# Kernel tuning notes

Measured on AMD Instinct MI355X. Metric: run time of the kernel, lower is better.

## Reference

```python
import jax, jax.numpy as jnp
import numpy as np

N_HEAD = 12


def setup_inputs() -> dict:
    key = jax.random.key(0)
    k1, k2, k3 = jax.random.split(key, 3)
    B, S, D = 4, 2048, 768
    x = jax.random.normal(k1, (B, S, D), dtype=jnp.float32)
    std = 0.02
    w_attn = jax.random.normal(k2, (D, 3 * D), dtype=jnp.float32) * std
    b_attn = jnp.zeros((3 * D,), dtype=jnp.float32)
    w_proj = jax.random.normal(k3, (D, D), dtype=jnp.float32) * std
    b_proj = jnp.zeros((D,), dtype=jnp.float32)
    return {"x": x, "w_attn": w_attn, "b_attn": b_attn,
            "w_proj": w_proj, "b_proj": b_proj}


def reference(x, w_attn, b_attn, w_proj, b_proj):
    B, S, D = x.shape
    H = N_HEAD
    hd = D // H
    # c_attn: [B,S,3D]
    qkv = jnp.einsum('bsd,de->bse', x, w_attn) + b_attn
    q, k, v = jnp.split(qkv, 3, axis=2)
    # split heads -> [B,H,S,hd]
    q = q.reshape(B, S, H, hd).transpose(0, 2, 1, 3)
    k = k.reshape(B, S, H, hd).transpose(0, 2, 1, 3)
    v = v.reshape(B, S, H, hd).transpose(0, 2, 1, 3)
    # scores [B,H,S,S]; scale=False in original default
    w = jnp.einsum('bhqd,bhkd->bhqk', q, k)
    # original mask trick: w*b + 1e-9*(1-b), b = lower-triangular ones
    mask = jnp.tril(jnp.ones((S, S), dtype=w.dtype))
    w = w * mask + 1e-9 * (1 - mask)
    w = jax.nn.softmax(w, axis=-1)
    a = jnp.einsum('bhqk,bhkd->bhqd', w, v)
    # merge heads -> [B,S,D]
    a = a.transpose(0, 2, 1, 3).reshape(B, S, D)
    # c_proj
    out = jnp.einsum('bsd,de->bse', a, w_proj) + b_proj
    return out
```

## Files before the change

kernel.cpp:

```cpp
#include <hip/hip_runtime.h>
#include <cstdint>

typedef unsigned short u16;
typedef __bf16 bf16;
typedef bf16 bf16x8 __attribute__((ext_vector_type(8)));
typedef u16 u16x4 __attribute__((ext_vector_type(4)));
typedef u16 u16x8 __attribute__((ext_vector_type(8)));
typedef float f32x4 __attribute__((ext_vector_type(4)));

__device__ __forceinline__ u16 f2b(float f) {
    return __builtin_bit_cast(u16, (bf16)f);
}
__device__ __forceinline__ float b2f(u16 u) {
    return __uint_as_float(((unsigned)u) << 16);
}
__device__ __forceinline__ void load_lds16(const void* g, void* l) {
    auto gp = reinterpret_cast<const __attribute__((address_space(1))) void*>(
        reinterpret_cast<uintptr_t>(g));
    auto lp = reinterpret_cast<__attribute__((address_space(3))) void*>(
        reinterpret_cast<uintptr_t>(l));
    __builtin_amdgcn_global_load_lds(gp, lp, 16, 0, 0);
}
__device__ __forceinline__ f32x4 mfma16(bf16x8 a, bf16x8 b, f32x4 c) {
    return __builtin_amdgcn_mfma_f32_16x16x32_bf16(a, b, c, 0, 0, 0);
}

__global__ __launch_bounds__(256) void convx_kernel(const float* __restrict__ x,
                                                    u16* __restrict__ xb, int n4) {
    int i = blockIdx.x * blockDim.x + threadIdx.x;
    int stride = gridDim.x * blockDim.x;
    for (; i < n4; i += stride) {
        float4 v = ((const float4*)x)[i];
        u16x4 r;
        r[0] = f2b(v.x); r[1] = f2b(v.y); r[2] = f2b(v.z); r[3] = f2b(v.w);
        *(u16x4*)&xb[(size_t)i * 4] = r;
    }
}

__global__ __launch_bounds__(256) void wtrans2_kernel(const float* __restrict__ wa,
                                                      const float* __restrict__ wp,
                                                      u16* __restrict__ wTa,
                                                      u16* __restrict__ wTp) {
    __shared__ float tile[32][33];
    const int bx = blockIdx.x;
    const float* w;
    u16* wT;
    int N, n0;
    if (bx < 72) { w = wa; wT = wTa; N = 2304; n0 = bx * 32; }
    else         { w = wp; wT = wTp; N = 768;  n0 = (bx - 72) * 32; }
    const int K = 768;
    int tx = threadIdx.x, ty = threadIdx.y;
    int k0 = blockIdx.y * 32;
#pragma unroll
    for (int i = 0; i < 4; ++i)
        tile[ty + i * 8][tx] = w[(size_t)(k0 + ty + i * 8) * N + n0 + tx];
    __syncthreads();
#pragma unroll
    for (int i = 0; i < 4; ++i)
        wT[(size_t)(n0 + ty + i * 8) * K + k0 + tx] = f2b(tile[tx][ty + i * 8]);
}

template <bool OUT_BF16>
__global__ __launch_bounds__(256, 3) void gemm_kernel(const u16* __restrict__ A,
                                                      const u16* __restrict__ Bt,
                                                      const float* __restrict__ bias,
                                                      void* __restrict__ out,
                                                      int M, int N, int K) {
    __shared__ __align__(16) u16 As[128 * 64];
    __shared__ __align__(16) u16 Bs[128 * 64];
    const int tid = threadIdx.x;
    const int wave = tid >> 6, lane = tid & 63;
    const int l15 = lane & 15, lg = lane >> 4;
    const int gx = gridDim.x;
    const int nwg = gx * gridDim.y;
    const int lin = blockIdx.y * gx + blockIdx.x;
    const int swz = (lin & 7) * (nwg >> 3) + (lin >> 3);
    const int tm = (swz / gx) * 128, tn = (swz % gx) * 128;
    const int wr = (wave >> 1) * 64, wc = (wave & 1) * 64;

    f32x4 acc[4][4] = {};

    const int rbase = wave * 8 + (lane >> 3);
    const int sslot = (lane & 7) ^ (rbase & 7);
    const u16* gA = A + (size_t)(tm + rbase) * K + sslot * 8;
    const u16* gB = Bt + (size_t)(tn + rbase) * K + sslot * 8;
    u16* ldsA = As + (size_t)(wave * 8) * 64;
    u16* ldsB = Bs + (size_t)(wave * 8) * 64;

    for (int kt = 0; kt < K; kt += 64) {
#pragma unroll
        for (int i = 0; i < 4; ++i) {
            load_lds16(gA + (size_t)i * 32 * K + kt, ldsA + i * 32 * 64);
            load_lds16(gB + (size_t)i * 32 * K + kt, ldsB + i * 32 * 64);
        }
        __syncthreads();
#pragma unroll
        for (int kk = 0; kk < 64; kk += 32) {
            const int sb = kk >> 3;
            bf16x8 af[4], bfr[4];
#pragma unroll
            for (int m = 0; m < 4; ++m) {
                int row = wr + m * 16 + l15;
                af[m] = *(const bf16x8*)&As[row * 64 + (((sb + lg) ^ (row & 7))) * 8];
            }
#pragma unroll
            for (int n = 0; n < 4; ++n) {
                int row = wc + n * 16 + l15;
                bfr[n] = *(const bf16x8*)&Bs[row * 64 + (((sb + lg) ^ (row & 7))) * 8];
            }
#pragma unroll
            for (int m = 0; m < 4; ++m)
#pragma unroll
                for (int n = 0; n < 4; ++n)
                    acc[m][n] = mfma16(af[m], bfr[n], acc[m][n]);
        }
        __syncthreads();
    }

#pragma unroll
    for (int n = 0; n < 4; ++n) {
        int col = tn + wc + n * 16 + l15;
        float bv = bias[col];
#pragma unroll
        for (int m = 0; m < 4; ++m) {
            int row0 = tm + wr + m * 16 + lg * 4;
#pragma unroll
            for (int r = 0; r < 4; ++r) {
                float v = acc[m][n][r] + bv;
                if constexpr (OUT_BF16)
                    ((u16*)out)[(size_t)(row0 + r) * N + col] = f2b(v);
                else
                    ((float*)out)[(size_t)(row0 + r) * N + col] = v;
            }
        }
    }
}

__global__ __launch_bounds__(256) void vtrans_kernel(const u16* __restrict__ qkv,
                                                     u16* __restrict__ vt,
                                                     float* __restrict__ ts_raw) {
    __shared__ __align__(16) u16 tile[64][72];
    __shared__ float red2[64][4];
    const int st = blockIdx.x, bh = blockIdx.y;
    const int b = bh / 12, h = bh % 12;
    const int t = threadIdx.x;
    const int sr = t >> 2, c4 = (t & 3) * 16;
    const u16* src = qkv + (size_t)(b * 2048 + st * 64 + sr) * 2304 + 1536 + h * 64 + c4;
    *(u16x8*)&tile[sr][c4] = *(const u16x8*)src;
    *(u16x8*)&tile[sr][c4 + 8] = *(const u16x8*)(src + 8);
    __syncthreads();
    const int dr = t >> 2, s4 = (t & 3) * 16;
    u16x8 w0, w1;
    float psum = 0.f;
#pragma unroll
    for (int j = 0; j < 8; ++j) {
        w0[j] = tile[s4 + j][dr];
        w1[j] = tile[s4 + 8 + j][dr];
        psum += b2f(w0[j]) + b2f(w1[j]);
    }
    u16* dst = vt + ((size_t)bh * 64 + dr) * 2048 + st * 64 + s4;
    *(u16x8*)dst = w0;
    *(u16x8*)(dst + 8) = w1;
    red2[dr][t & 3] = psum;
    __syncthreads();
    if (t < 64)
        ts_raw[((size_t)bh * 32 + st) * 64 + t] =
            red2[t][0] + red2[t][1] + red2[t][2] + red2[t][3];
}

__global__ __launch_bounds__(256, 5) void attn_kernel(const u16* __restrict__ qkv,
                                                      const u16* __restrict__ vt,
                                                      const float* __restrict__ ts_raw,
                                                      u16* __restrict__ aout) {
    __shared__ __align__(16) u16 Ks[2][64 * 64];
    __shared__ __align__(16) u16 Vs[2][64 * 64];
    const int bh = blockIdx.x;
    const int qt = 31 - blockIdx.y;
    const int b = bh / 12, h = bh % 12;
    const int tid = threadIdx.x, wave = tid >> 6, lane = tid & 63;
    const int l15 = lane & 15, lg = lane >> 4;
    const int q0 = qt * 64 + wave * 16;
    const size_t rowbase = (size_t)b * 2048;

    bf16x8 qf[2];
#pragma unroll
    for (int ks = 0; ks < 2; ++ks)
        qf[ks] = *(const bf16x8*)(qkv + (rowbase + q0 + l15) * 2304 + h * 64 +
                                  ks * 32 + lg * 8);

    f32x4 o[4] = {};
    float mrun = -1e30f;
    float lrun = 0.f;

    const int rbase = wave * 8 + (lane >> 3);
    const int sslot = (lane & 7) ^ (rbase & 7);
    const int sig0 = ((rbase & 0x1C) << 1) | (rbase & 3);
    const u16* gK = qkv + (rowbase + sig0) * 2304 + 768 + h * 64 + sslot * 8;
    const u16* gV = vt + ((size_t)bh * 64 + rbase) * 2048 + sslot * 8;
    const int ldsoff = wave * 8 * 64;

    const int nkt = qt + 1;
#pragma unroll
    for (int i = 0; i < 2; ++i) {
        load_lds16(gK + (size_t)(i * 4) * 2304, &Ks[0][ldsoff + i * 32 * 64]);
        load_lds16(gV + (size_t)(i * 32) * 2048, &Vs[0][ldsoff + i * 32 * 64]);
    }

    for (int kt = 0; kt < nkt; ++kt) {
        __syncthreads();
        const int cur = kt & 1;
        if (kt + 1 < nkt) {
            const int nx = cur ^ 1;
#pragma unroll
            for (int i = 0; i < 2; ++i) {
                load_lds16(gK + (size_t)((kt + 1) * 64 + i * 4) * 2304,
                           &Ks[nx][ldsoff + i * 32 * 64]);
                load_lds16(gV + (size_t)(i * 32) * 2048 + (kt + 1) * 64,
                           &Vs[nx][ldsoff + i * 32 * 64]);
            }
        }

        f32x4 sacc[4] = {};
        __builtin_amdgcn_s_setprio(1);
#pragma unroll
        for (int ks = 0; ks < 2; ++ks) {
#pragma unroll
            for (int n = 0; n < 4; ++n) {
                int row = n * 16 + l15;
                bf16x8 ak = *(const bf16x8*)&Ks[cur][row * 64 +
                                                     (((ks * 4 + lg) ^ (row & 7))) * 8];
                sacc[n] = mfma16(ak, qf[ks], sacc[n]);
            }
        }
        __builtin_amdgcn_s_setprio(0);

        if (kt == qt) {
            const int q = q0 + l15;
            const int kb = kt * 64 + lg * 8;
#pragma unroll
            for (int n = 0; n < 4; ++n) {
                const int kn = kb + (n & 1) * 32 + ((n >> 1) << 2);
#pragma unroll
                for (int r = 0; r < 4; ++r)
                    if (kn + r > q) sacc[n][r] = 1e-9f;
            }
        }

        float mx = fmaxf(fmaxf(sacc[0][0], sacc[0][1]), fmaxf(sacc[0][2], sacc[0][3]));
#pragma unroll
        for (int n = 1; n < 4; ++n)
            mx = fmaxf(mx, fmaxf(fmaxf(sacc[n][0], sacc[n][1]),
                                 fmaxf(sacc[n][2], sacc[n][3])));
        if (__any(mx > mrun + 8.0f)) {
            float rm = fmaxf(mx, __shfl_xor(mx, 16));
            rm = fmaxf(rm, __shfl_xor(rm, 32));
            const float mnew = fmaxf(mrun, rm);
            const float alpha = __expf(mrun - mnew);
            mrun = mnew;
            lrun *= alpha;
#pragma unroll
            for (int dn = 0; dn < 4; ++dn) o[dn] *= alpha;
        }

#pragma unroll
        for (int n = 0; n < 4; ++n)
#pragma unroll
            for (int r = 0; r < 4; ++r) {
                float p = __expf(sacc[n][r] - mrun);
                lrun += p;
                sacc[n][r] = p;
            }
        bf16x8 bp0, bp1;
#pragma unroll
        for (int j = 0; j < 4; ++j) {
            bp0[j]     = (bf16)sacc[0][j];
            bp0[j + 4] = (bf16)sacc[2][j];
            bp1[j]     = (bf16)sacc[1][j];
            bp1[j + 4] = (bf16)sacc[3][j];
        }

        __builtin_amdgcn_s_setprio(1);
#pragma unroll
        for (int ks = 0; ks < 2; ++ks) {
            bf16x8 bp = ks ? bp1 : bp0;
#pragma unroll
            for (int dn = 0; dn < 4; ++dn) {
                int row = dn * 16 + l15;
                bf16x8 av = *(const bf16x8*)&Vs[cur][row * 64 +
                                                     (((ks * 4 + lg) ^ (row & 7))) * 8];
                o[dn] = mfma16(av, bp, o[dn]);
            }
        }
        __builtin_amdgcn_s_setprio(0);
    }

    lrun += __shfl_xor(lrun, 16);
    lrun += __shfl_xor(lrun, 32);

    if (qt < 31) {
        const float nf = (float)((31 - qt) * 64);
        const float mnew = fmaxf(mrun, 1e-9f);
        const float a = __expf(mrun - mnew);
        const float c = __expf(1e-9f - mnew);
        lrun = lrun * a + nf * c;
        f32x4 suf[4] = {};
        for (int t = qt + 1; t < 32; ++t) {
            const float* sp = ts_raw + ((size_t)bh * 32 + t) * 64;
#pragma unroll
            for (int dn = 0; dn < 4; ++dn)
                suf[dn] += *(const f32x4*)&sp[dn * 16 + lg * 4];
        }
#pragma unroll
        for (int dn = 0; dn < 4; ++dn)
            o[dn] = o[dn] * a + suf[dn] * c;
    }

    const float inv = 1.f / lrun;
    const size_t row = rowbase + q0 + l15;
#pragma unroll
    for (int dn = 0; dn < 4; ++dn) {
        u16x4 st;
#pragma unroll
        for (int r = 0; r < 4; ++r) st[r] = f2b(o[dn][r] * inv);
        *(u16x4*)&aout[row * 768 + h * 64 + dn * 16 + lg * 4] = st;
    }
}

extern "C" void kernel_launch(void* const* d_in, const int* in_sizes, int n_in,
                              void* d_out, int out_size, void* d_ws, size_t ws_size,
                              hipStream_t stream) {
    const float* x      = (const float*)d_in[0];
    const float* w_attn = (const float*)d_in[1];
    const float* b_attn = (const float*)d_in[2];
    const float* w_proj = (const float*)d_in[3];
    const float* b_proj = (const float*)d_in[4];
    float* out = (float*)d_out;
    char* ws = (char*)d_ws;

    u16* xb      = (u16*)(ws + 0);
    u16* wTa     = (u16*)(ws + 12582912);
    u16* wTp     = (u16*)(ws + 16121856);
    u16* qkv     = (u16*)(ws + 17301504);
    u16* vt      = (u16*)(ws + 55050240);
    u16* aout    = (u16*)(ws + 67633152);
    float* ts_raw = (float*)(ws + 0);

    convx_kernel<<<dim3(2048), dim3(256), 0, stream>>>(x, xb, 8192 * 768 / 4);
    wtrans2_kernel<<<dim3(96, 24), dim3(32, 8), 0, stream>>>(w_attn, w_proj, wTa, wTp);
    gemm_kernel<true><<<dim3(18, 64), dim3(256), 0, stream>>>(xb, wTa, b_attn,
                                                              (void*)qkv, 8192, 2304, 768);
    vtrans_kernel<<<dim3(32, 48), dim3(256), 0, stream>>>(qkv, vt, ts_raw);
    attn_kernel<<<dim3(48, 32), dim3(256), 0, stream>>>(qkv, vt, ts_raw, aout);
    gemm_kernel<false><<<dim3(6, 64), dim3(256), 0, stream>>>(aout, wTp, b_proj,
                                                              (void*)out, 8192, 768, 768);
}
```

Baseline: 201.9 us.

## Double-buffer GEMM LDS tiles and vectorize epilogue stores via swapped MFMA operands

The GEMM kernel now keeps two LDS stages for A and B and prefetches the next K tile with global_load_lds while the MFMAs run on the current one. This hides global load latency and removes one barrier per iteration. The MFMA operands are swapped so each lane holds four consecutive output columns, which allows vectorized bias loads and 8- or 16-byte stores instead of scalar strided stores. LDS use per block doubles, so the occupancy hint drops from 3 to 2 blocks per CU.

```diff
diff --git a/kernel.cpp b/kernel.cpp
--- a/kernel.cpp
+++ b/kernel.cpp
@@ -61,13 +61,12 @@
 }
 
 template <bool OUT_BF16>
-__global__ __launch_bounds__(256, 3) void gemm_kernel(const u16* __restrict__ A,
+__global__ __launch_bounds__(256, 2) void gemm_kernel(const u16* __restrict__ A,
                                                       const u16* __restrict__ Bt,
                                                       const float* __restrict__ bias,
                                                       void* __restrict__ out,
                                                       int M, int N, int K) {
-    __shared__ __align__(16) u16 As[128 * 64];
-    __shared__ __align__(16) u16 Bs[128 * 64];
+    __shared__ __align__(16) u16 SMEM[4 * 128 * 64];
     const int tid = threadIdx.x;
     const int wave = tid >> 6, lane = tid & 63;
     const int l15 = lane & 15, lg = lane >> 4;
@@ -84,16 +83,29 @@
     const int sslot = (lane & 7) ^ (rbase & 7);
     const u16* gA = A + (size_t)(tm + rbase) * K + sslot * 8;
     const u16* gB = Bt + (size_t)(tn + rbase) * K + sslot * 8;
-    u16* ldsA = As + (size_t)(wave * 8) * 64;
-    u16* ldsB = Bs + (size_t)(wave * 8) * 64;
-
-    for (int kt = 0; kt < K; kt += 64) {
-#pragma unroll
-        for (int i = 0; i < 4; ++i) {
-            load_lds16(gA + (size_t)i * 32 * K + kt, ldsA + i * 32 * 64);
-            load_lds16(gB + (size_t)i * 32 * K + kt, ldsB + i * 32 * 64);
-        }
+    const int woff = wave * 8 * 64;
+    const int nkt = K >> 6;
+
+#pragma unroll
+    for (int i = 0; i < 4; ++i) {
+        load_lds16(gA + (size_t)i * 32 * K, SMEM + woff + i * 32 * 64);
+        load_lds16(gB + (size_t)i * 32 * K, SMEM + 8192 + woff + i * 32 * 64);
+    }
+
+    for (int kt = 0; kt < nkt; ++kt) {
         __syncthreads();
+        const int cur = kt & 1;
+        if (kt + 1 < nkt) {
+            u16* ldsA = SMEM + (cur ^ 1) * 2 * 8192 + woff;
+            u16* ldsB = ldsA + 8192;
+#pragma unroll
+            for (int i = 0; i < 4; ++i) {
+                load_lds16(gA + (size_t)i * 32 * K + (kt + 1) * 64, ldsA + i * 32 * 64);
+                load_lds16(gB + (size_t)i * 32 * K + (kt + 1) * 64, ldsB + i * 32 * 64);
+            }
+        }
+        const u16* As = SMEM + cur * 2 * 8192;
+        const u16* Bs = As + 8192;
 #pragma unroll
         for (int kk = 0; kk < 64; kk += 32) {
             const int sb = kk >> 3;
@@ -112,25 +124,24 @@
             for (int m = 0; m < 4; ++m)
 #pragma unroll
                 for (int n = 0; n < 4; ++n)
-                    acc[m][n] = mfma16(af[m], bfr[n], acc[m][n]);
-        }
-        __syncthreads();
-    }
-
-#pragma unroll
-    for (int n = 0; n < 4; ++n) {
-        int col = tn + wc + n * 16 + l15;
-        float bv = bias[col];
-#pragma unroll
-        for (int m = 0; m < 4; ++m) {
-            int row0 = tm + wr + m * 16 + lg * 4;
-#pragma unroll
-            for (int r = 0; r < 4; ++r) {
-                float v = acc[m][n][r] + bv;
-                if constexpr (OUT_BF16)
-                    ((u16*)out)[(size_t)(row0 + r) * N + col] = f2b(v);
-                else
-                    ((float*)out)[(size_t)(row0 + r) * N + col] = v;
+                    acc[m][n] = mfma16(bfr[n], af[m], acc[m][n]);
+        }
+    }
+
+#pragma unroll
+    for (int m = 0; m < 4; ++m) {
+        const size_t row = (size_t)(tm + wr + m * 16 + l15);
+#pragma unroll
+        for (int n = 0; n < 4; ++n) {
+            const int col = tn + wc + n * 16 + lg * 4;
+            f32x4 v = acc[m][n] + *(const f32x4*)&bias[col];
+            if constexpr (OUT_BF16) {
+                u16x4 pk;
+#pragma unroll
+                for (int r = 0; r < 4; ++r) pk[r] = f2b(v[r]);
+                *(u16x4*)&((u16*)out)[row * N + col] = pk;
+            } else {
+                *(f32x4*)&((float*)out)[row * N + col] = v;
             }
         }
     }
```

Result: slower. 210.9 us (+4.5%).
